# Kernel optimization log

Measured on AMD Instinct MI355X. Metric: run time of the kernel, lower is better.

## Reference

```python
import jax, jax.numpy as jnp
import numpy as np

I16_MIN, I16_MAX = -32768, 32767
NUM_SEG = 8


def setup_inputs() -> dict:
    key = jax.random.key(0)
    k1, k2, k3, k4, k5, k6 = jax.random.split(key, 6)
    # Float activation; quantized to qint16 inside the op via input_scale.
    x = jax.random.normal(k1, (16, 1024, 2048), dtype=jnp.float32)
    input_scale = jnp.full((1,), 1.0 / 8192.0, dtype=jnp.float32)  # randn*8192 spans most of int16
    out_scale = jnp.full((1,), 1e-3, dtype=jnp.float32)
    # Per-segment fixed-point linear coefficients (as produced by _convert_linear_kb / toqint):
    # 16-bit k, wide b pre-shifted by left_shift, result right-shifted by right_shift.
    alpha = jax.random.randint(k2, (NUM_SEG,), -4096, 4096, dtype=jnp.int32)        # int16 k
    beta = jax.random.randint(k3, (NUM_SEG,), -(1 << 20), 1 << 20, dtype=jnp.int32)  # int b
    left_shift = jax.random.randint(k4, (NUM_SEG,), 0, 5, dtype=jnp.int32)           # int8 shift
    right_shift = jax.random.randint(k5, (NUM_SEG,), 1, 15, dtype=jnp.int32)         # int8 shift
    # Sorted segment upper bounds in quantized domain; last entry pinned to qint16 max
    # (mirrors `segment_max[-1] = info.max` in _init_multi_table_params).
    segment_max = jnp.sort(jax.random.randint(k6, (NUM_SEG,), I16_MIN, I16_MAX, dtype=jnp.int32))
    segment_max = segment_max.at[-1].set(I16_MAX)
    return dict(x=x, input_scale=input_scale, out_scale=out_scale, alpha=alpha,
                beta=beta, left_shift=left_shift, right_shift=right_shift,
                segment_max=segment_max)


def reference(x, input_scale, out_scale, alpha, beta, left_shift, right_shift, segment_max):
    # Quantize input to qint16 (scale-only, zero_point = 0 as in the module).
    xi = jnp.clip(jnp.round(x / input_scale), I16_MIN, I16_MAX).astype(jnp.int32)
    # Segment selection: element belongs to the first segment whose upper bound >= xi.
    idx = jnp.clip(jnp.searchsorted(segment_max, xi, side='left'), 0, NUM_SEG - 1)
    # Gather per-segment fixed-point coefficients.
    k = alpha[idx]
    b = beta[idx]
    ls = left_shift[idx]
    rs = right_shift[idx]
    # Hardware shift-multiply-add: acc = k*x + (b << left_shift), then rounded
    # arithmetic right shift by right_shift, saturate to qint16.
    acc = k * xi + jnp.left_shift(b, ls)
    round_bias = jnp.where(rs > 0, jnp.left_shift(jnp.int32(1), jnp.maximum(rs - 1, 0)), jnp.int32(0))
    qy = jnp.clip(jnp.right_shift(acc + round_bias, rs), I16_MIN, I16_MAX)
    # Dequantized output (QTensor data * out_scale, zero_point = 0).
    return qy.astype(jnp.float32) * out_scale
```

## Files before the change

kernel.cpp:

```cpp
#include <hip/hip_runtime.h>


__device__ __forceinline__ float seg_one(float x, float inv_s,
                                         float sm0, float sm1, float sm2, float sm3,
                                         float sm4, float sm5, float sm6,
                                         const float2* tab, float olo, float ohi)
{
    float xf = rintf(x * inv_s);
    xf = fminf(fmaxf(xf, -32768.0f), 32767.0f);
    int idx = (sm0 < xf) + (sm1 < xf) + (sm2 < xf) + (sm3 < xf)
            + (sm4 < xf) + (sm5 < xf) + (sm6 < xf);
    float2 t = tab[idx];
    float y = fmaf(t.x, xf, t.y);
    return fminf(fmaxf(y, olo), ohi);
}

__global__ __launch_bounds__(256) void SegmentLUT_83021717831949_kernel(
    const float* __restrict__ x,
    const float* __restrict__ input_scale,
    const float* __restrict__ out_scale,
    const int*   __restrict__ alpha,
    const int*   __restrict__ beta,
    const int*   __restrict__ lsh,
    const int*   __restrict__ rsh,
    const int*   __restrict__ smax,
    float*       __restrict__ out,
    int n)
{
    __shared__ float2 tab[8];
    float os = out_scale[0];
    if (threadIdx.x < 8) {
        int j  = (int)threadIdx.x;
        int rs = rsh[j];
        int rm1 = rs - 1 > 0 ? rs - 1 : 0;
        int rbias = rs > 0 ? (1 << rm1) : 0;
        int bc = (int)((unsigned)beta[j] << (lsh[j] & 31)) + rbias;
        float sc = ldexpf(os, -rs);
        tab[j] = make_float2((float)alpha[j] * sc, (float)bc * sc);
    }
    float s     = input_scale[0];
    float inv_s = 1.0f / s;
    float sm0 = (float)smax[0], sm1 = (float)smax[1], sm2 = (float)smax[2];
    float sm3 = (float)smax[3], sm4 = (float)smax[4], sm5 = (float)smax[5];
    float sm6 = (float)smax[6];
    float olo = -32768.0f * os, ohi = 32767.0f * os;
    __syncthreads();

    int nvec   = n >> 2;
    int stride = (int)(gridDim.x * blockDim.x);
    int tid    = (int)(blockIdx.x * blockDim.x + threadIdx.x);

    const float4* __restrict__ xv = (const float4*)x;
    float4* __restrict__ ov = (float4*)out;

    int i = tid;
    for (; i + stride < nvec; i += 2 * stride) {
        float4 a = xv[i];
        float4 b = xv[i + stride];
        float4 oa, ob;
        oa.x = seg_one(a.x, inv_s, sm0, sm1, sm2, sm3, sm4, sm5, sm6, tab, olo, ohi);
        oa.y = seg_one(a.y, inv_s, sm0, sm1, sm2, sm3, sm4, sm5, sm6, tab, olo, ohi);
        oa.z = seg_one(a.z, inv_s, sm0, sm1, sm2, sm3, sm4, sm5, sm6, tab, olo, ohi);
        oa.w = seg_one(a.w, inv_s, sm0, sm1, sm2, sm3, sm4, sm5, sm6, tab, olo, ohi);
        ob.x = seg_one(b.x, inv_s, sm0, sm1, sm2, sm3, sm4, sm5, sm6, tab, olo, ohi);
        ob.y = seg_one(b.y, inv_s, sm0, sm1, sm2, sm3, sm4, sm5, sm6, tab, olo, ohi);
        ob.z = seg_one(b.z, inv_s, sm0, sm1, sm2, sm3, sm4, sm5, sm6, tab, olo, ohi);
        ob.w = seg_one(b.w, inv_s, sm0, sm1, sm2, sm3, sm4, sm5, sm6, tab, olo, ohi);
        ov[i] = oa;
        ov[i + stride] = ob;
    }
    for (; i < nvec; i += stride) {
        float4 a = xv[i];
        float4 oa;
        oa.x = seg_one(a.x, inv_s, sm0, sm1, sm2, sm3, sm4, sm5, sm6, tab, olo, ohi);
        oa.y = seg_one(a.y, inv_s, sm0, sm1, sm2, sm3, sm4, sm5, sm6, tab, olo, ohi);
        oa.z = seg_one(a.z, inv_s, sm0, sm1, sm2, sm3, sm4, sm5, sm6, tab, olo, ohi);
        oa.w = seg_one(a.w, inv_s, sm0, sm1, sm2, sm3, sm4, sm5, sm6, tab, olo, ohi);
        ov[i] = oa;
    }
    for (int k = (nvec << 2) + tid; k < n; k += stride) {
        out[k] = seg_one(x[k], inv_s, sm0, sm1, sm2, sm3, sm4, sm5, sm6, tab, olo, ohi);
    }
}

extern "C" void kernel_launch(void* const* d_in, const int* in_sizes, int n_in,
                              void* d_out, int out_size, void* d_ws, size_t ws_size,
                              hipStream_t stream) {
    const float* x           = (const float*)d_in[0];
    const float* input_scale = (const float*)d_in[1];
    const float* out_scale   = (const float*)d_in[2];
    const int*   alpha       = (const int*)d_in[3];
    const int*   beta        = (const int*)d_in[4];
    const int*   lsh         = (const int*)d_in[5];
    const int*   rsh         = (const int*)d_in[6];
    const int*   smax        = (const int*)d_in[7];
    float* out = (float*)d_out;

    int n = in_sizes[0];
    int nvec = n >> 2;
    int blocks = (nvec + 255) / 256;
    if (blocks > 2048) blocks = 2048;
    if (blocks < 1) blocks = 1;

    SegmentLUT_83021717831949_kernel<<<blocks, 256, 0, stream>>>(
        x, input_scale, out_scale, alpha, beta, lsh, rsh, smax, out, n);
}
```

Measured before the change: 245.3 us.

## Unroll grid-stride loop to four vectors with nontemporal stores and fmed3 clamps

Raises the grid-stride unroll from two to four float4 loads per iteration, writes outputs with nontemporal stores to avoid polluting cache on a streaming write, and replaces min/max clamp pairs with single fmed3 instructions. The aim is more memory-level parallelism and cheaper ALU work in this bandwidth-bound elementwise kernel. Extra unrolling raises register use, and with a 2048-block cap some threads may fall into the remainder loop more often.

```diff
diff --git a/kernel.cpp b/kernel.cpp
--- a/kernel.cpp
+++ b/kernel.cpp
@@ -1,5 +1,7 @@
 #include <hip/hip_runtime.h>
 
+
+typedef float f32x4 __attribute__((ext_vector_type(4)));
 
 __device__ __forceinline__ float seg_one(float x, float inv_s,
                                          float sm0, float sm1, float sm2, float sm3,
@@ -7,12 +9,12 @@
                                          const float2* tab, float olo, float ohi)
 {
     float xf = rintf(x * inv_s);
-    xf = fminf(fmaxf(xf, -32768.0f), 32767.0f);
+    xf = __builtin_amdgcn_fmed3f(xf, -32768.0f, 32767.0f);
     int idx = (sm0 < xf) + (sm1 < xf) + (sm2 < xf) + (sm3 < xf)
             + (sm4 < xf) + (sm5 < xf) + (sm6 < xf);
     float2 t = tab[idx];
     float y = fmaf(t.x, xf, t.y);
-    return fminf(fmaxf(y, olo), ohi);
+    return __builtin_amdgcn_fmed3f(y, olo, ohi);
 }
 
 __global__ __launch_bounds__(256) void SegmentLUT_83021717831949_kernel(
@@ -38,8 +40,7 @@
         float sc = ldexpf(os, -rs);
         tab[j] = make_float2((float)alpha[j] * sc, (float)bc * sc);
     }
-    float s     = input_scale[0];
-    float inv_s = 1.0f / s;
+    float inv_s = 1.0f / input_scale[0];
     float sm0 = (float)smax[0], sm1 = (float)smax[1], sm2 = (float)smax[2];
     float sm3 = (float)smax[3], sm4 = (float)smax[4], sm5 = (float)smax[5];
     float sm6 = (float)smax[6];
@@ -50,37 +51,41 @@
     int stride = (int)(gridDim.x * blockDim.x);
     int tid    = (int)(blockIdx.x * blockDim.x + threadIdx.x);
 
-    const float4* __restrict__ xv = (const float4*)x;
-    float4* __restrict__ ov = (float4*)out;
+    const f32x4* __restrict__ xv = (const f32x4*)x;
+    f32x4* __restrict__ ov = (f32x4*)out;
+
+#define SEG1(e) seg_one((e), inv_s, sm0, sm1, sm2, sm3, sm4, sm5, sm6, tab, olo, ohi)
+#define SEG4(o, v) do { \
+        (o).x = SEG1((v).x); (o).y = SEG1((v).y); \
+        (o).z = SEG1((v).z); (o).w = SEG1((v).w); } while (0)
 
     int i = tid;
-    for (; i + stride < nvec; i += 2 * stride) {
-        float4 a = xv[i];
-        float4 b = xv[i + stride];
-        float4 oa, ob;
-        oa.x = seg_one(a.x, inv_s, sm0, sm1, sm2, sm3, sm4, sm5, sm6, tab, olo, ohi);
-        oa.y = seg_one(a.y, inv_s, sm0, sm1, sm2, sm3, sm4, sm5, sm6, tab, olo, ohi);
-        oa.z = seg_one(a.z, inv_s, sm0, sm1, sm2, sm3, sm4, sm5, sm6, tab, olo, ohi);
-        oa.w = seg_one(a.w, inv_s, sm0, sm1, sm2, sm3, sm4, sm5, sm6, tab, olo, ohi);
-        ob.x = seg_one(b.x, inv_s, sm0, sm1, sm2, sm3, sm4, sm5, sm6, tab, olo, ohi);
-        ob.y = seg_one(b.y, inv_s, sm0, sm1, sm2, sm3, sm4, sm5, sm6, tab, olo, ohi);
-        ob.z = seg_one(b.z, inv_s, sm0, sm1, sm2, sm3, sm4, sm5, sm6, tab, olo, ohi);
-        ob.w = seg_one(b.w, inv_s, sm0, sm1, sm2, sm3, sm4, sm5, sm6, tab, olo, ohi);
-        ov[i] = oa;
-        ov[i + stride] = ob;
+    for (; i + 3 * stride < nvec; i += 4 * stride) {
+        f32x4 v0 = xv[i];
+        f32x4 v1 = xv[i + stride];
+        f32x4 v2 = xv[i + 2 * stride];
+        f32x4 v3 = xv[i + 3 * stride];
+        f32x4 o0, o1, o2, o3;
+        SEG4(o0, v0);
+        SEG4(o1, v1);
+        SEG4(o2, v2);
+        SEG4(o3, v3);
+        __builtin_nontemporal_store(o0, &ov[i]);
+        __builtin_nontemporal_store(o1, &ov[i + stride]);
+        __builtin_nontemporal_store(o2, &ov[i + 2 * stride]);
+        __builtin_nontemporal_store(o3, &ov[i + 3 * stride]);
     }
     for (; i < nvec; i += stride) {
-        float4 a = xv[i];
-        float4 oa;
-        oa.x = seg_one(a.x, inv_s, sm0, sm1, sm2, sm3, sm4, sm5, sm6, tab, olo, ohi);
-        oa.y = seg_one(a.y, inv_s, sm0, sm1, sm2, sm3, sm4, sm5, sm6, tab, olo, ohi);
-        oa.z = seg_one(a.z, inv_s, sm0, sm1, sm2, sm3, sm4, sm5, sm6, tab, olo, ohi);
-        oa.w = seg_one(a.w, inv_s, sm0, sm1, sm2, sm3, sm4, sm5, sm6, tab, olo, ohi);
-        ov[i] = oa;
+        f32x4 v = xv[i];
+        f32x4 o;
+        SEG4(o, v);
+        __builtin_nontemporal_store(o, &ov[i]);
     }
     for (int k = (nvec << 2) + tid; k < n; k += stride) {
-        out[k] = seg_one(x[k], inv_s, sm0, sm1, sm2, sm3, sm4, sm5, sm6, tab, olo, ohi);
+        out[k] = SEG1(x[k]);
     }
+#undef SEG4
+#undef SEG1
 }
 
 extern "C" void kernel_launch(void* const* d_in, const int* in_sizes, int n_in,
```

Result: slower. 251.1 us (+2.4%).
